# Performance work log

Measured on AMD Instinct MI355X. Metric: run time of the kernel, lower is better.

The kernel has to match this reference:

```python
import jax, jax.numpy as jnp
import numpy as np

N, E, H, D_IN, D_EDGE, L = 20000, 320000, 128, 128, 32, 4
EPS = 1e-5

def setup_inputs() -> dict:
    key = jax.random.key(0)
    ks = jax.random.split(key, 16)
    d_in_edge = 2 * H + 1 + D_EDGE  # cat[h_row, h_col, radial, edge_attr] (input_nf==hidden here)
    s = 0.02
    inp = {
        'h': jax.random.normal(ks[0], (N, D_IN), jnp.float32),
        'coords': jax.random.normal(ks[1], (N, 3), jnp.float32),
        'edge_attr': jax.random.normal(ks[2], (E, D_EDGE), jnp.float32),
        'edges': jax.random.randint(ks[3], (2, E), 0, N),
        'edge_w1': jax.random.normal(ks[4], (L, d_in_edge, H), jnp.float32) * s,
        'edge_b1': jnp.zeros((L, H), jnp.float32),
        'edge_w2': jax.random.normal(ks[5], (L, H, H), jnp.float32) * s,
        'edge_b2': jnp.zeros((L, H), jnp.float32),
        'node_w1': jax.random.normal(ks[6], (L, H + H, H), jnp.float32) * s,
        'node_b1': jnp.zeros((L, H), jnp.float32),
        'node_w2': jax.random.normal(ks[7], (L, H, H), jnp.float32) * s,
        'node_b2': jnp.zeros((L, H), jnp.float32),
        'ln_g': jnp.ones((H,), jnp.float32),
        'ln_b': jnp.zeros((H,), jnp.float32),
    }
    return inp

def _egnn(h, coords, edge_attr, edges, ew1, eb1, ew2, eb2, nw1, nb1, nw2, nb2, ln_g, ln_b):
    row, col = edges[0], edges[1]
    # squared-distance radial feature; coords are not updated across layers
    # (EGNN.forward discards coordinate updates: h, _, _ = layer(...)).
    diff = coords[row] - coords[col]              # [E,3]
    radial = jnp.sum(diff * diff, axis=-1, keepdims=True)  # [E,1]
    for i in range(L):
        hr, hc = h[row], h[col]                   # gathers [E,H]
        m = jnp.concatenate([hr, hc, radial, edge_attr], axis=-1)
        m = jax.nn.silu(m @ ew1[i] + eb1[i])      # [E,H]
        m = jax.nn.silu(m @ ew2[i] + eb2[i])      # [E,H]
        agg = jax.ops.segment_sum(m, row, num_segments=N)  # scatter-add [N,H]
        z = jnp.concatenate([h, agg], axis=-1)    # [N,2H]
        out = jax.nn.silu(z @ nw1[i] + nb1[i]) @ nw2[i] + nb2[i]
        h = out if i == 0 else h + out            # layer 0 non-recurrent
    mu = jnp.mean(h, axis=-1, keepdims=True)
    var = jnp.mean((h - mu) ** 2, axis=-1, keepdims=True)
    return (h - mu) * jax.lax.rsqrt(var + EPS) * ln_g + ln_b

def reference(h, coords, edge_attr, edges, edge_w1, edge_b1, edge_w2, edge_b2,
              node_w1, node_b1, node_w2, node_b2, ln_g, ln_b):
    return _egnn(h, coords, edge_attr, edges, edge_w1, edge_b1, edge_w2, edge_b2,
                 node_w1, node_b1, node_w2, node_b2, ln_g, ln_b)
```

## Files before the change

### kernel.cpp

```cpp
#include <hip/hip_runtime.h>
#include <hip/hip_bf16.h>

#define NN 20000
#define EE 320000
#define HH 128
#define DE 32
#define LL 4

typedef __bf16 bf16_t;
typedef __bf16 bf16x8 __attribute__((ext_vector_type(8)));
typedef __bf16 bf16x4 __attribute__((ext_vector_type(4)));
typedef float f32x4 __attribute__((ext_vector_type(4)));

static __device__ __forceinline__ float silu_f(float x) {
    return x * __builtin_amdgcn_rcpf(1.f + __expf(-x));
}

static __device__ __forceinline__ int permrow(int el) {
    return ((el >> 2) & 3) * 16 + ((el >> 4) & 3) * 4 + (el & 3);
}

__global__ void prep_weights(const float* __restrict__ ew1, const float* __restrict__ eb1f,
                             const float* __restrict__ ew2,
                             const float* __restrict__ nw1, const float* __restrict__ nw2,
                             bf16_t* __restrict__ WPT, bf16_t* __restrict__ W1C,
                             bf16_t* __restrict__ W2T, bf16_t* __restrict__ N1T,
                             bf16_t* __restrict__ N2T)
{
    int i = blockIdx.x * 256 + threadIdx.x;
    const int SW = LL * 256 * 128;
    if (i < SW) {
        int l = i / (256 * 128), r = i % (256 * 128);
        int c = r / 128, k = r % 128;
        int krow = (c < 128) ? k : 128 + k;
        WPT[i] = (bf16_t)ew1[((size_t)l * 289 + krow) * 128 + (c & 127)];
        return;
    }
    i -= SW;
    const int SC = LL * 128 * 64;
    if (i < SC) {
        int l = i / (128 * 64), r = i % (128 * 64);
        int c = r / 64, kk = r % 64;
        float v;
        if (kk == 0)       v = ew1[((size_t)l * 289 + 256) * 128 + c];
        else if (kk <= 32) v = ew1[((size_t)l * 289 + 256 + kk) * 128 + c];
        else if (kk == 33) v = eb1f[l * 128 + c];
        else               v = 0.f;
        W1C[i] = (bf16_t)v;
        return;
    }
    i -= SC;
    const int S2 = LL * 128 * 128;
    if (i < S2) {
        int l = i / (128 * 128), r = i % (128 * 128);
        int n = r / 128, k = r % 128;
        W2T[i] = (bf16_t)ew2[((size_t)l * 128 + k) * 128 + n];
        return;
    }
    i -= S2;
    const int S3 = LL * 128 * 256;
    if (i < S3) {
        int l = i / (128 * 256), r = i % (128 * 256);
        int n = r / 256, k = r % 256;
        N1T[i] = (bf16_t)nw1[((size_t)l * 256 + k) * 128 + n];
        return;
    }
    i -= S3;
    if (i < S2) {
        int l = i / (128 * 128), r = i % (128 * 128);
        int n = r / 128, k = r % 128;
        N2T[i] = (bf16_t)nw2[((size_t)l * 128 + k) * 128 + n];
    }
}

__global__ void hist_kernel(const int* __restrict__ edges, int* __restrict__ counts)
{
    int e = blockIdx.x * 256 + threadIdx.x;
    if (e < EE) atomicAdd(&counts[edges[e]], 1);
}

__global__ void scan_kernel(const int* __restrict__ counts, int* __restrict__ starts)
{
    __shared__ int wsum[16];
    __shared__ int running_s;
    const int tid = threadIdx.x;
    const int lane = tid & 63, wv = tid >> 6;
    if (tid == 0) running_s = 0;
    __syncthreads();
    for (int base = 0; base < NN; base += 1024) {
        int i = base + tid;
        int v = (i < NN) ? counts[i] : 0;
        int orig = v;
        #pragma unroll
        for (int off = 1; off < 64; off <<= 1) {
            int t = __shfl_up(v, off);
            if (lane >= off) v += t;
        }
        if (lane == 63) wsum[wv] = v;
        __syncthreads();
        if (tid < 16) {
            int s = wsum[tid];
            #pragma unroll
            for (int off = 1; off < 16; off <<= 1) {
                int t = __shfl_up(s, off);
                if (tid >= off) s += t;
            }
            wsum[tid] = s;
        }
        __syncthreads();
        int waveoff = (wv == 0) ? 0 : wsum[wv - 1];
        if (i < NN) starts[i] = running_s + waveoff + v - orig;
        int total = wsum[15];
        __syncthreads();
        if (tid == 0) running_s += total;
        __syncthreads();
    }
}

__global__ void scatter_kernel(const int* __restrict__ edges, int* __restrict__ cursor,
                               int* __restrict__ eidx, int* __restrict__ row_s,
                               int* __restrict__ col_s)
{
    int e = blockIdx.x * 256 + threadIdx.x;
    if (e >= EE) return;
    int r = edges[e], c = edges[EE + e];
    int pos = atomicAdd(&cursor[r], 1);
    eidx[pos] = e;
    row_s[pos] = r;
    col_s[pos] = c;
}

__global__ void build_re(const int* __restrict__ eidx, const int* __restrict__ row_s,
                         const int* __restrict__ col_s, const float* __restrict__ coords,
                         const float* __restrict__ ea, bf16_t* __restrict__ RE)
{
    int pos = blockIdx.x * 256 + threadIdx.x;
    if (pos >= EE) return;
    int e = eidx[pos], r = row_s[pos], c = col_s[pos];
    float dx = coords[r * 3 + 0] - coords[c * 3 + 0];
    float dy = coords[r * 3 + 1] - coords[c * 3 + 1];
    float dz = coords[r * 3 + 2] - coords[c * 3 + 2];
    alignas(16) bf16_t buf[40];
    buf[0] = (bf16_t)(dx * dx + dy * dy + dz * dz);
    #pragma unroll
    for (int j = 0; j < 32; ++j) buf[1 + j] = (bf16_t)ea[(size_t)e * DE + j];
    buf[33] = (bf16_t)1.0f;
    #pragma unroll
    for (int j = 34; j < 40; ++j) buf[j] = (bf16_t)0.f;
    bf16x8* dst = (bf16x8*)(RE + (size_t)pos * 40);
    #pragma unroll
    for (int k = 0; k < 5; ++k) dst[k] = ((const bf16x8*)buf)[k];
}

__global__ __launch_bounds__(256, 2) void node_pre(
    const float* __restrict__ h, const bf16_t* __restrict__ WPT,
    bf16_t* __restrict__ P, int layer)
{
    __shared__ bf16_t Hs[64][136];
    const int tid = threadIdx.x;
    const int n0 = blockIdx.x * 64;
    {
        const int nl = tid >> 2, q = tid & 3;
        const int node = n0 + nl;
        if (node < NN) {
            const float* hp = h + (size_t)node * HH;
            #pragma unroll
            for (int j = 0; j < 8; ++j) {
                float4 v = *(const float4*)(hp + q * 32 + j * 4);
                int k = q * 32 + j * 4;
                Hs[nl][k + 0] = (bf16_t)v.x; Hs[nl][k + 1] = (bf16_t)v.y;
                Hs[nl][k + 2] = (bf16_t)v.z; Hs[nl][k + 3] = (bf16_t)v.w;
            }
        } else {
            #pragma unroll
            for (int j = 0; j < 8; ++j) {
                int k = q * 32 + j * 4;
                Hs[nl][k] = (bf16_t)0.f; Hs[nl][k + 1] = (bf16_t)0.f;
                Hs[nl][k + 2] = (bf16_t)0.f; Hs[nl][k + 3] = (bf16_t)0.f;
            }
        }
    }
    __syncthreads();

    const int lane = tid & 63, w = tid >> 6;
    const int ln = lane & 15, kg = lane >> 4;

    f32x4 acc[4][4] = {};
    const bf16_t* Wl = WPT + (size_t)layer * 256 * 128;
    #pragma unroll
    for (int kt = 0; kt < 4; ++kt) {
        const int kb = kt * 32 + kg * 8;
        bf16x8 a[4], b[4];
        #pragma unroll
        for (int m = 0; m < 4; ++m) a[m] = *(const bf16x8*)&Hs[m * 16 + ln][kb];
        #pragma unroll
        for (int n = 0; n < 4; ++n)
            b[n] = *(const bf16x8*)(Wl + (size_t)(w * 64 + n * 16 + ln) * 128 + kb);
        #pragma unroll
        for (int m = 0; m < 4; ++m)
            #pragma unroll
            for (int n = 0; n < 4; ++n)
                acc[m][n] = __builtin_amdgcn_mfma_f32_16x16x32_bf16(a[m], b[n], acc[m][n], 0, 0, 0);
    }
    #pragma unroll
    for (int n = 0; n < 4; ++n) {
        int col = w * 64 + n * 16 + ln;
        #pragma unroll
        for (int m = 0; m < 4; ++m)
            #pragma unroll
            for (int rr = 0; rr < 4; ++rr) {
                int node = n0 + m * 16 + kg * 4 + rr;
                if (node < NN) P[(size_t)node * 256 + col] = (bf16_t)acc[m][n][rr];
            }
    }
}

__global__ __launch_bounds__(256, 6) void edge_kernel(
    const bf16_t* __restrict__ P, const bf16_t* __restrict__ RE,
    const int* __restrict__ row_s, const int* __restrict__ col_s,
    const bf16_t* __restrict__ W1C, const bf16_t* __restrict__ W2T,
    const float* __restrict__ b2, float* __restrict__ agg, int layer)
{
    __shared__ bf16_t pABs[64][136];
    __shared__ bf16_t REb[64][72];

    const int tid = threadIdx.x;
    const int e0 = blockIdx.x * 64;

    {
        const int el = tid >> 2, q = tid & 3;
        const int es = e0 + permrow(el);
        const bf16_t* src = RE + (size_t)es * 40;
        bf16x8 z = {};
        if (q < 2) {
            *(bf16x8*)&REb[el][q * 16]     = *(const bf16x8*)(src + q * 16);
            *(bf16x8*)&REb[el][q * 16 + 8] = *(const bf16x8*)(src + q * 16 + 8);
        } else if (q == 2) {
            *(bf16x8*)&REb[el][32] = *(const bf16x8*)(src + 32);
            *(bf16x8*)&REb[el][40] = z;
        } else {
            *(bf16x8*)&REb[el][48] = z;
            *(bf16x8*)&REb[el][56] = z;
        }
    }
    {
        const int el = tid >> 2, q = tid & 3;
        const int es = e0 + permrow(el);
        int r = row_s[es], c = col_s[es];
        const bf16_t* pa = P + (size_t)r * 256 + q * 32;
        const bf16_t* pb = P + (size_t)c * 256 + 128 + q * 32;
        #pragma unroll
        for (int j = 0; j < 4; ++j) {
            bf16x8 va = *(const bf16x8*)(pa + j * 8);
            bf16x8 vb = *(const bf16x8*)(pb + j * 8);
            bf16x8 o;
            #pragma unroll
            for (int t = 0; t < 8; ++t) o[t] = (bf16_t)((float)va[t] + (float)vb[t]);
            *(bf16x8*)&pABs[el][q * 32 + j * 8] = o;
        }
    }
    __syncthreads();

    const int lane = tid & 63, w = tid >> 6;
    const int ln = lane & 15, kg = lane >> 4;

    f32x4 acc[2][4] = {};
    const bf16_t* W1l = W1C + (size_t)layer * 128 * 64;
    #pragma unroll
    for (int kt = 0; kt < 2; ++kt) {
        const int kb = kt * 32 + kg * 8;
        bf16x8 aW[2], bR[4];
        #pragma unroll
        for (int oc = 0; oc < 2; ++oc)
            aW[oc] = *(const bf16x8*)(W1l + (size_t)(w * 32 + oc * 16 + ln) * 64 + kb);
        #pragma unroll
        for (int e = 0; e < 4; ++e) bR[e] = *(const bf16x8*)&REb[e * 16 + ln][kb];
        #pragma unroll
        for (int oc = 0; oc < 2; ++oc)
            #pragma unroll
            for (int e = 0; e < 4; ++e)
                acc[oc][e] = __builtin_amdgcn_mfma_f32_16x16x32_bf16(aW[oc], bR[e], acc[oc][e], 0, 0, 0);
    }

    #pragma unroll
    for (int oc = 0; oc < 2; ++oc) {
        const int ob = w * 32 + oc * 16 + kg * 4;
        #pragma unroll
        for (int e = 0; e < 4; ++e) {
            const int er = e * 16 + ln;
            bf16x4 pv = *(const bf16x4*)&pABs[er][ob];
            bf16x4 o;
            #pragma unroll
            for (int r = 0; r < 4; ++r)
                o[r] = (bf16_t)silu_f(acc[oc][e][r] + (float)pv[r]);
            *(bf16x4*)&pABs[er][ob] = o;
        }
    }
    __syncthreads();

    f32x4 acc2[4][2] = {};
    const bf16_t* W2l = W2T + (size_t)layer * 128 * 128;
    #pragma unroll
    for (int kt = 0; kt < 4; ++kt) {
        const int kb = kt * 32 + kg * 8;
        bf16x8 a[4], b[2];
        #pragma unroll
        for (int m = 0; m < 4; ++m) a[m] = *(const bf16x8*)&pABs[m * 16 + ln][kb];
        #pragma unroll
        for (int n = 0; n < 2; ++n)
            b[n] = *(const bf16x8*)(W2l + (size_t)(w * 32 + n * 16 + ln) * 128 + kb);
        #pragma unroll
        for (int m = 0; m < 4; ++m)
            #pragma unroll
            for (int n = 0; n < 2; ++n)
                acc2[m][n] = __builtin_amdgcn_mfma_f32_16x16x32_bf16(a[m], b[n], acc2[m][n], 0, 0, 0);
    }

    {
        int myrow[16];
        {
            const int4* rp = (const int4*)(row_s + e0 + kg * 16);
            #pragma unroll
            for (int j = 0; j < 4; ++j) {
                int4 v = rp[j];
                myrow[j * 4 + 0] = v.x; myrow[j * 4 + 1] = v.y;
                myrow[j * 4 + 2] = v.z; myrow[j * 4 + 3] = v.w;
            }
        }

        #pragma unroll
        for (int n = 0; n < 2; ++n) {
            int col = w * 32 + n * 16 + ln;
            float bias = b2[layer * 128 + col];
            float s = 0.f;
            int cur = myrow[0];
            #pragma unroll
            for (int m = 0; m < 4; ++m) {
                #pragma unroll
                for (int rr = 0; rr < 4; ++rr) {
                    int r = myrow[m * 4 + rr];
                    float v = silu_f(acc2[m][n][rr] + bias);
                    if (r != cur) {
                        atomicAdd(&agg[(size_t)cur * HH + col], s);
                        s = 0.f; cur = r;
                    }
                    s += v;
                }
            }
            atomicAdd(&agg[(size_t)cur * HH + col], s);
        }
    }
}

__global__ __launch_bounds__(256, 2) void node_fused(
    const float* __restrict__ hin, float* __restrict__ hout,
    const float* __restrict__ agg,
    const bf16_t* __restrict__ N1T, const float* __restrict__ b1,
    const bf16_t* __restrict__ N2T, const float* __restrict__ b2,
    const bf16_t* __restrict__ WPT, bf16_t* __restrict__ P,
    int layer, int produceP)
{
    __shared__ bf16_t Zs[64][264];
    __shared__ bf16_t M1s[64][136];

    const int tid = threadIdx.x;
    const int n0 = blockIdx.x * 64;

    {
        const int nl = tid >> 2, q = tid & 3;
        const int node = n0 + nl;
        if (node < NN) {
            const float* hp = hin + (size_t)node * HH;
            const float* ap = agg + (size_t)node * HH;
            #pragma unroll
            for (int kk = 0; kk < 64; kk += 4) {
                int k = q * 64 + kk;
                float4 v = (k < 128) ? *(const float4*)(hp + k)
                                     : *(const float4*)(ap + (k - 128));
                Zs[nl][k + 0] = (bf16_t)v.x; Zs[nl][k + 1] = (bf16_t)v.y;
                Zs[nl][k + 2] = (bf16_t)v.z; Zs[nl][k + 3] = (bf16_t)v.w;
            }
        } else {
            #pragma unroll
            for (int kk = 0; kk < 64; kk += 4) {
                int k = q * 64 + kk;
                Zs[nl][k + 0] = (bf16_t)0.f; Zs[nl][k + 1] = (bf16_t)0.f;
                Zs[nl][k + 2] = (bf16_t)0.f; Zs[nl][k + 3] = (bf16_t)0.f;
            }
        }
    }
    __syncthreads();

    const int lane = tid & 63, w = tid >> 6;
    const int ln = lane & 15, kg = lane >> 4;

    f32x4 acc[2][4] = {};
    const bf16_t* N1l = N1T + (size_t)layer * 128 * 256;
    #pragma unroll
    for (int kt = 0; kt < 8; ++kt) {
        const int kb = kt * 32 + kg * 8;
        bf16x8 aW[2], bZ[4];
        #pragma unroll
        for (int oc = 0; oc < 2; ++oc)
            aW[oc] = *(const bf16x8*)(N1l + (size_t)(w * 32 + oc * 16 + ln) * 256 + kb);
        #pragma unroll
        for (int e = 0; e < 4; ++e) bZ[e] = *(const bf16x8*)&Zs[e * 16 + ln][kb];
        #pragma unroll
        for (int oc = 0; oc < 2; ++oc)
            #pragma unroll
            for (int e = 0; e < 4; ++e)
                acc[oc][e] = __builtin_amdgcn_mfma_f32_16x16x32_bf16(aW[oc], bZ[e], acc[oc][e], 0, 0, 0);
    }

    #pragma unroll
    for (int oc = 0; oc < 2; ++oc) {
        const int ob = w * 32 + oc * 16 + kg * 4;
        const float4 b14 = *(const float4*)&b1[layer * 128 + ob];
        #pragma unroll
        for (int e = 0; e < 4; ++e) {
            const int nd = e * 16 + ln;
            bf16x4 o;
            o[0] = (bf16_t)silu_f(acc[oc][e][0] + b14.x);
            o[1] = (bf16_t)silu_f(acc[oc][e][1] + b14.y);
            o[2] = (bf16_t)silu_f(acc[oc][e][2] + b14.z);
            o[3] = (bf16_t)silu_f(acc[oc][e][3] + b14.w);
            *(bf16x4*)&M1s[nd][ob] = o;
        }
    }
    __syncthreads();

    f32x4 acc2[2][4] = {};
    const bf16_t* N2l = N2T + (size_t)layer * 128 * 128;
    #pragma unroll
    for (int kt = 0; kt < 4; ++kt) {
        const int kb = kt * 32 + kg * 8;
        bf16x8 aW[2], bM[4];
        #pragma unroll
        for (int oc = 0; oc < 2; ++oc)
            aW[oc] = *(const bf16x8*)(N2l + (size_t)(w * 32 + oc * 16 + ln) * 128 + kb);
        #pragma unroll
        for (int e = 0; e < 4; ++e) bM[e] = *(const bf16x8*)&M1s[e * 16 + ln][kb];
        #pragma unroll
        for (int oc = 0; oc < 2; ++oc)
            #pragma unroll
            for (int e = 0; e < 4; ++e)
                acc2[oc][e] = __builtin_amdgcn_mfma_f32_16x16x32_bf16(aW[oc], bM[e], acc2[oc][e], 0, 0, 0);
    }

    #pragma unroll
    for (int oc = 0; oc < 2; ++oc) {
        const int ob = w * 32 + oc * 16 + kg * 4;
        const float4 b24 = *(const float4*)&b2[layer * 128 + ob];
        #pragma unroll
        for (int e = 0; e < 4; ++e) {
            const int ndl = e * 16 + ln;
            const int node = n0 + ndl;
            float x0 = acc2[oc][e][0] + b24.x;
            float x1 = acc2[oc][e][1] + b24.y;
            float x2 = acc2[oc][e][2] + b24.z;
            float x3 = acc2[oc][e][3] + b24.w;
            if (node < NN) {
                if (layer != 0) {
                    float4 hv = *(const float4*)&hin[(size_t)node * HH + ob];
                    x0 += hv.x; x1 += hv.y; x2 += hv.z; x3 += hv.w;
                }
                float4 ov; ov.x = x0; ov.y = x1; ov.z = x2; ov.w = x3;
                *(float4*)&hout[(size_t)node * HH + ob] = ov;
            }
            bf16x4 z;
            z[0] = (bf16_t)x0; z[1] = (bf16_t)x1;
            z[2] = (bf16_t)x2; z[3] = (bf16_t)x3;
            *(bf16x4*)&Zs[ndl][ob] = z;
        }
    }

    if (produceP) {
        __syncthreads();
        f32x4 accP[4][4] = {};
        const bf16_t* Wl = WPT + (size_t)(layer + 1) * 256 * 128;
        #pragma unroll
        for (int kt = 0; kt < 4; ++kt) {
            const int kb = kt * 32 + kg * 8;
            bf16x8 aW[4], bZ[4];
            #pragma unroll
            for (int oc = 0; oc < 4; ++oc)
                aW[oc] = *(const bf16x8*)(Wl + (size_t)(w * 64 + oc * 16 + ln) * 128 + kb);
            #pragma unroll
            for (int e = 0; e < 4; ++e) bZ[e] = *(const bf16x8*)&Zs[e * 16 + ln][kb];
            #pragma unroll
            for (int oc = 0; oc < 4; ++oc)
                #pragma unroll
                for (int e = 0; e < 4; ++e)
                    accP[oc][e] = __builtin_amdgcn_mfma_f32_16x16x32_bf16(aW[oc], bZ[e], accP[oc][e], 0, 0, 0);
        }
        #pragma unroll
        for (int oc = 0; oc < 4; ++oc) {
            const int pb = w * 64 + oc * 16 + kg * 4;
            #pragma unroll
            for (int e = 0; e < 4; ++e) {
                const int node = n0 + e * 16 + ln;
                if (node < NN) {
                    bf16x4 o;
                    o[0] = (bf16_t)accP[oc][e][0]; o[1] = (bf16_t)accP[oc][e][1];
                    o[2] = (bf16_t)accP[oc][e][2]; o[3] = (bf16_t)accP[oc][e][3];
                    *(bf16x4*)&P[(size_t)node * 256 + pb] = o;
                }
            }
        }
    }
}

__global__ void ln_kernel(float* __restrict__ h, const float* __restrict__ g,
                          const float* __restrict__ bb)
{
    int node = blockIdx.x * 4 + (threadIdx.x >> 6);
    int lane = threadIdx.x & 63;
    if (node >= NN) return;
    float* hp = h + (size_t)node * HH;
    float v0 = hp[lane], v1 = hp[lane + 64];
    float s = v0 + v1, sq = v0 * v0 + v1 * v1;
    #pragma unroll
    for (int o = 32; o; o >>= 1) {
        s  += __shfl_xor(s, o);
        sq += __shfl_xor(sq, o);
    }
    float mu  = s * (1.f / 128.f);
    float var = sq * (1.f / 128.f) - mu * mu;
    float inv = rsqrtf(var + 1e-5f);
    hp[lane]      = (v0 - mu) * inv * g[lane]      + bb[lane];
    hp[lane + 64] = (v1 - mu) * inv * g[lane + 64] + bb[lane + 64];
}

extern "C" void kernel_launch(void* const* d_in, const int* in_sizes, int n_in,
                              void* d_out, int out_size, void* d_ws, size_t ws_size,
                              hipStream_t stream)
{
    (void)in_sizes; (void)n_in; (void)out_size; (void)ws_size;

    const float* h_in    = (const float*)d_in[0];
    const float* coords  = (const float*)d_in[1];
    const float* ea      = (const float*)d_in[2];
    const int*   edges   = (const int*)d_in[3];
    const float* ew1     = (const float*)d_in[4];
    const float* eb1     = (const float*)d_in[5];
    const float* ew2     = (const float*)d_in[6];
    const float* eb2     = (const float*)d_in[7];
    const float* nw1     = (const float*)d_in[8];
    const float* nb1     = (const float*)d_in[9];
    const float* nw2     = (const float*)d_in[10];
    const float* nb2     = (const float*)d_in[11];
    const float* ln_g    = (const float*)d_in[12];
    const float* ln_b    = (const float*)d_in[13];

    char* ws = (char*)d_ws;
    int*    counts = (int*)(ws + 0);
    int*    starts = (int*)(ws + 80128);
    int*    cursor = (int*)(ws + 160384);
    int*    eidx   = (int*)(ws + 240512);
    int*    row_s  = (int*)(ws + 1520512);
    int*    col_s  = (int*)(ws + 2800512);
    bf16_t* RE     = (bf16_t*)(ws + 4080512);
    bf16_t* P      = (bf16_t*)(ws + 29680512);
    float*  agg    = (float*)(ws + 39920512);
    bf16_t* WPT    = (bf16_t*)(ws + 50160512);
    bf16_t* W1C    = (bf16_t*)(ws + 50422656);
    bf16_t* W2T    = (bf16_t*)(ws + 50488192);
    bf16_t* N1T    = (bf16_t*)(ws + 50619264);
    bf16_t* N2T    = (bf16_t*)(ws + 50881408);

    float* h = (float*)d_out;

    prep_weights<<<1664, 256, 0, stream>>>(ew1, eb1, ew2, nw1, nw2,
                                           WPT, W1C, W2T, N1T, N2T);

    hipMemsetAsync(counts, 0, NN * sizeof(int), stream);
    hist_kernel<<<(EE + 255) / 256, 256, 0, stream>>>(edges, counts);
    scan_kernel<<<1, 1024, 0, stream>>>(counts, starts);
    hipMemcpyAsync(cursor, starts, NN * sizeof(int),
                   hipMemcpyDeviceToDevice, stream);
    scatter_kernel<<<(EE + 255) / 256, 256, 0, stream>>>(edges, cursor, eidx, row_s, col_s);
    build_re<<<(EE + 255) / 256, 256, 0, stream>>>(eidx, row_s, col_s, coords, ea, RE);

    node_pre<<<(NN + 63) / 64, 256, 0, stream>>>(h_in, WPT, P, 0);

    for (int l = 0; l < LL; ++l) {
        hipMemsetAsync(agg, 0, (size_t)NN * HH * sizeof(float), stream);
        edge_kernel<<<EE / 64, 256, 0, stream>>>(P, RE, row_s, col_s,
                                                 W1C, W2T, eb2, agg, l);
        node_fused<<<(NN + 63) / 64, 256, 0, stream>>>(
            (l == 0) ? h_in : h, h, agg, N1T, nb1, N2T, nb2,
            WPT, P, l, (l < LL - 1) ? 1 : 0);
    }
    ln_kernel<<<NN / 4, 256, 0, stream>>>(h, ln_g, ln_b);
}
```

Measured before the change: 432.1 us.

## Load edge gathers directly into MFMA accumulators and halve node tile size

The edge kernel stops staging the gathered P rows and the RE edge features through shared memory. Each lane now loads its P[row]+P[col] slice straight into the accumulator registers as the initial value, and reads RE operands from global memory. This removes a shared-memory staging pass and a barrier, at the cost of narrower (8-byte) uncoalesced gathers and a lower occupancy hint. The node kernel moves from 64 to 32 nodes per block, doubling the grid for more parallelism, and drops its bounds checks because NN divides evenly by 32.

```diff
diff --git a/kernel.cpp b/kernel.cpp
--- a/kernel.cpp
+++ b/kernel.cpp
@@ -14,10 +14,6 @@
 
 static __device__ __forceinline__ float silu_f(float x) {
     return x * __builtin_amdgcn_rcpf(1.f + __expf(-x));
-}
-
-static __device__ __forceinline__ int permrow(int el) {
-    return ((el >> 2) & 3) * 16 + ((el >> 4) & 3) * 4 + (el & 3);
 }
 
 __global__ void prep_weights(const float* __restrict__ ew1, const float* __restrict__ eb1f,
@@ -215,56 +211,41 @@
     }
 }
 
-__global__ __launch_bounds__(256, 6) void edge_kernel(
+__global__ __launch_bounds__(256, 4) void edge_kernel(
     const bf16_t* __restrict__ P, const bf16_t* __restrict__ RE,
     const int* __restrict__ row_s, const int* __restrict__ col_s,
     const bf16_t* __restrict__ W1C, const bf16_t* __restrict__ W2T,
     const float* __restrict__ b2, float* __restrict__ agg, int layer)
 {
-    __shared__ bf16_t pABs[64][136];
-    __shared__ bf16_t REb[64][72];
+    __shared__ bf16_t M1s[64][136];
 
     const int tid = threadIdx.x;
     const int e0 = blockIdx.x * 64;
-
-    {
-        const int el = tid >> 2, q = tid & 3;
-        const int es = e0 + permrow(el);
-        const bf16_t* src = RE + (size_t)es * 40;
-        bf16x8 z = {};
-        if (q < 2) {
-            *(bf16x8*)&REb[el][q * 16]     = *(const bf16x8*)(src + q * 16);
-            *(bf16x8*)&REb[el][q * 16 + 8] = *(const bf16x8*)(src + q * 16 + 8);
-        } else if (q == 2) {
-            *(bf16x8*)&REb[el][32] = *(const bf16x8*)(src + 32);
-            *(bf16x8*)&REb[el][40] = z;
-        } else {
-            *(bf16x8*)&REb[el][48] = z;
-            *(bf16x8*)&REb[el][56] = z;
-        }
-    }
-    {
-        const int el = tid >> 2, q = tid & 3;
-        const int es = e0 + permrow(el);
-        int r = row_s[es], c = col_s[es];
-        const bf16_t* pa = P + (size_t)r * 256 + q * 32;
-        const bf16_t* pb = P + (size_t)c * 256 + 128 + q * 32;
-        #pragma unroll
-        for (int j = 0; j < 4; ++j) {
-            bf16x8 va = *(const bf16x8*)(pa + j * 8);
-            bf16x8 vb = *(const bf16x8*)(pb + j * 8);
-            bf16x8 o;
-            #pragma unroll
-            for (int t = 0; t < 8; ++t) o[t] = (bf16_t)((float)va[t] + (float)vb[t]);
-            *(bf16x8*)&pABs[el][q * 32 + j * 8] = o;
-        }
-    }
-    __syncthreads();
-
     const int lane = tid & 63, w = tid >> 6;
     const int ln = lane & 15, kg = lane >> 4;
 
-    f32x4 acc[2][4] = {};
+    int p[4];
+    #pragma unroll
+    for (int e = 0; e < 4; ++e)
+        p[e] = e0 + ((ln >> 2) * 16) + e * 4 + (ln & 3);
+
+    f32x4 acc[2][4];
+    #pragma unroll
+    for (int e = 0; e < 4; ++e) {
+        int r = row_s[p[e]], c = col_s[p[e]];
+        const bf16_t* pa = P + (size_t)r * 256;
+        const bf16_t* pb = P + (size_t)c * 256 + 128;
+        #pragma unroll
+        for (int oc = 0; oc < 2; ++oc) {
+            const int ob = w * 32 + oc * 16 + kg * 4;
+            bf16x4 va = *(const bf16x4*)(pa + ob);
+            bf16x4 vb = *(const bf16x4*)(pb + ob);
+            #pragma unroll
+            for (int j = 0; j < 4; ++j)
+                acc[oc][e][j] = (float)va[j] + (float)vb[j];
+        }
+    }
+
     const bf16_t* W1l = W1C + (size_t)layer * 128 * 64;
     #pragma unroll
     for (int kt = 0; kt < 2; ++kt) {
@@ -274,7 +255,8 @@
         for (int oc = 0; oc < 2; ++oc)
             aW[oc] = *(const bf16x8*)(W1l + (size_t)(w * 32 + oc * 16 + ln) * 64 + kb);
         #pragma unroll
-        for (int e = 0; e < 4; ++e) bR[e] = *(const bf16x8*)&REb[e * 16 + ln][kb];
+        for (int e = 0; e < 4; ++e)
+            bR[e] = *(const bf16x8*)(RE + (size_t)p[e] * 40 + kb);
         #pragma unroll
         for (int oc = 0; oc < 2; ++oc)
             #pragma unroll
@@ -287,13 +269,11 @@
         const int ob = w * 32 + oc * 16 + kg * 4;
         #pragma unroll
         for (int e = 0; e < 4; ++e) {
-            const int er = e * 16 + ln;
-            bf16x4 pv = *(const bf16x4*)&pABs[er][ob];
             bf16x4 o;
             #pragma unroll
-            for (int r = 0; r < 4; ++r)
-                o[r] = (bf16_t)silu_f(acc[oc][e][r] + (float)pv[r]);
-            *(bf16x4*)&pABs[er][ob] = o;
+            for (int j = 0; j < 4; ++j)
+                o[j] = (bf16_t)silu_f(acc[oc][e][j]);
+            *(bf16x4*)&M1s[e * 16 + ln][ob] = o;
         }
     }
     __syncthreads();
@@ -305,7 +285,7 @@
         const int kb = kt * 32 + kg * 8;
         bf16x8 a[4], b[2];
         #pragma unroll
-        for (int m = 0; m < 4; ++m) a[m] = *(const bf16x8*)&pABs[m * 16 + ln][kb];
+        for (int m = 0; m < 4; ++m) a[m] = *(const bf16x8*)&M1s[m * 16 + ln][kb];
         #pragma unroll
         for (int n = 0; n < 2; ++n)
             b[n] = *(const bf16x8*)(W2l + (size_t)(w * 32 + n * 16 + ln) * 128 + kb);
@@ -352,7 +332,7 @@
     }
 }
 
-__global__ __launch_bounds__(256, 2) void node_fused(
+__global__ __launch_bounds__(256, 4) void node_fused(
     const float* __restrict__ hin, float* __restrict__ hout,
     const float* __restrict__ agg,
     const bf16_t* __restrict__ N1T, const float* __restrict__ b1,
@@ -360,33 +340,24 @@
     const bf16_t* __restrict__ WPT, bf16_t* __restrict__ P,
     int layer, int produceP)
 {
-    __shared__ bf16_t Zs[64][264];
-    __shared__ bf16_t M1s[64][136];
+    __shared__ bf16_t Zs[32][264];
+    __shared__ bf16_t M1s[32][136];
 
     const int tid = threadIdx.x;
-    const int n0 = blockIdx.x * 64;
+    const int n0 = blockIdx.x * 32;
 
     {
-        const int nl = tid >> 2, q = tid & 3;
+        const int nl = tid >> 3, q = tid & 7;
         const int node = n0 + nl;
-        if (node < NN) {
-            const float* hp = hin + (size_t)node * HH;
-            const float* ap = agg + (size_t)node * HH;
-            #pragma unroll
-            for (int kk = 0; kk < 64; kk += 4) {
-                int k = q * 64 + kk;
-                float4 v = (k < 128) ? *(const float4*)(hp + k)
-                                     : *(const float4*)(ap + (k - 128));
-                Zs[nl][k + 0] = (bf16_t)v.x; Zs[nl][k + 1] = (bf16_t)v.y;
-                Zs[nl][k + 2] = (bf16_t)v.z; Zs[nl][k + 3] = (bf16_t)v.w;
-            }
-        } else {
-            #pragma unroll
-            for (int kk = 0; kk < 64; kk += 4) {
-                int k = q * 64 + kk;
-                Zs[nl][k + 0] = (bf16_t)0.f; Zs[nl][k + 1] = (bf16_t)0.f;
-                Zs[nl][k + 2] = (bf16_t)0.f; Zs[nl][k + 3] = (bf16_t)0.f;
-            }
+        const float* hp = hin + (size_t)node * HH;
+        const float* ap = agg + (size_t)node * HH;
+        #pragma unroll
+        for (int kk = 0; kk < 32; kk += 4) {
+            int k = q * 32 + kk;
+            float4 v = (k < 128) ? *(const float4*)(hp + k)
+                                 : *(const float4*)(ap + (k - 128));
+            Zs[nl][k + 0] = (bf16_t)v.x; Zs[nl][k + 1] = (bf16_t)v.y;
+            Zs[nl][k + 2] = (bf16_t)v.z; Zs[nl][k + 3] = (bf16_t)v.w;
         }
     }
     __syncthreads();
@@ -394,21 +365,21 @@
     const int lane = tid & 63, w = tid >> 6;
     const int ln = lane & 15, kg = lane >> 4;
 
-    f32x4 acc[2][4] = {};
+    f32x4 acc[2][2] = {};
     const bf16_t* N1l = N1T + (size_t)layer * 128 * 256;
     #pragma unroll
     for (int kt = 0; kt < 8; ++kt) {
         const int kb = kt * 32 + kg * 8;
-        bf16x8 aW[2], bZ[4];
+        bf16x8 aW[2], bZ[2];
         #pragma unroll
         for (int oc = 0; oc < 2; ++oc)
             aW[oc] = *(const bf16x8*)(N1l + (size_t)(w * 32 + oc * 16 + ln) * 256 + kb);
         #pragma unroll
-        for (int e = 0; e < 4; ++e) bZ[e] = *(const bf16x8*)&Zs[e * 16 + ln][kb];
+        for (int e = 0; e < 2; ++e) bZ[e] = *(const bf16x8*)&Zs[e * 16 + ln][kb];
         #pragma unroll
         for (int oc = 0; oc < 2; ++oc)
             #pragma unroll
-            for (int e = 0; e < 4; ++e)
+            for (int e = 0; e < 2; ++e)
                 acc[oc][e] = __builtin_amdgcn_mfma_f32_16x16x32_bf16(aW[oc], bZ[e], acc[oc][e], 0, 0, 0);
     }
 
@@ -417,7 +388,7 @@
         const int ob = w * 32 + oc * 16 + kg * 4;
         const float4 b14 = *(const float4*)&b1[layer * 128 + ob];
         #pragma unroll
-        for (int e = 0; e < 4; ++e) {
+        for (int e = 0; e < 2; ++e) {
             const int nd = e * 16 + ln;
             bf16x4 o;
             o[0] = (bf16_t)silu_f(acc[oc][e][0] + b14.x);
@@ -429,21 +400,21 @@
     }
     __syncthreads();
 
-    f32x4 acc2[2][4] = {};
+    f32x4 acc2[2][2] = {};
     const bf16_t* N2l = N2T + (size_t)layer * 128 * 128;
     #pragma unroll
     for (int kt = 0; kt < 4; ++kt) {
         const int kb = kt * 32 + kg * 8;
-        bf16x8 aW[2], bM[4];
+        bf16x8 aW[2], bM[2];
         #pragma unroll
         for (int oc = 0; oc < 2; ++oc)
             aW[oc] = *(const bf16x8*)(N2l + (size_t)(w * 32 + oc * 16 + ln) * 128 + kb);
         #pragma unroll
-        for (int e = 0; e < 4; ++e) bM[e] = *(const bf16x8*)&M1s[e * 16 + ln][kb];
+        for (int e = 0; e < 2; ++e) bM[e] = *(const bf16x8*)&M1s[e * 16 + ln][kb];
         #pragma unroll
         for (int oc = 0; oc < 2; ++oc)
             #pragma unroll
-            for (int e = 0; e < 4; ++e)
+            for (int e = 0; e < 2; ++e)
                 acc2[oc][e] = __builtin_amdgcn_mfma_f32_16x16x32_bf16(aW[oc], bM[e], acc2[oc][e], 0, 0, 0);
     }
 
@@ -452,21 +423,19 @@
         const int ob = w * 32 + oc * 16 + kg * 4;
         const float4 b24 = *(const float4*)&b2[layer * 128 + ob];
         #pragma unroll
-        for (int e = 0; e < 4; ++e) {
+        for (int e = 0; e < 2; ++e) {
             const int ndl = e * 16 + ln;
             const int node = n0 + ndl;
             float x0 = acc2[oc][e][0] + b24.x;
             float x1 = acc2[oc][e][1] + b24.y;
             float x2 = acc2[oc][e][2] + b24.z;
             float x3 = acc2[oc][e][3] + b24.w;
-            if (node < NN) {
-                if (layer != 0) {
-                    float4 hv = *(const float4*)&hin[(size_t)node * HH + ob];
-                    x0 += hv.x; x1 += hv.y; x2 += hv.z; x3 += hv.w;
-                }
-                float4 ov; ov.x = x0; ov.y = x1; ov.z = x2; ov.w = x3;
-                *(float4*)&hout[(size_t)node * HH + ob] = ov;
-            }
+            if (layer != 0) {
+                float4 hv = *(const float4*)&hin[(size_t)node * HH + ob];
+                x0 += hv.x; x1 += hv.y; x2 += hv.z; x3 += hv.w;
+            }
+            float4 ov; ov.x = x0; ov.y = x1; ov.z = x2; ov.w = x3;
+            *(float4*)&hout[(size_t)node * HH + ob] = ov;
             bf16x4 z;
             z[0] = (bf16_t)x0; z[1] = (bf16_t)x1;
             z[2] = (bf16_t)x2; z[3] = (bf16_t)x3;
@@ -476,35 +445,33 @@
 
     if (produceP) {
         __syncthreads();
-        f32x4 accP[4][4] = {};
+        f32x4 accP[4][2] = {};
         const bf16_t* Wl = WPT + (size_t)(layer + 1) * 256 * 128;
         #pragma unroll
         for (int kt = 0; kt < 4; ++kt) {
             const int kb = kt * 32 + kg * 8;
-            bf16x8 aW[4], bZ[4];
+            bf16x8 aW[4], bZ[2];
             #pragma unroll
             for (int oc = 0; oc < 4; ++oc)
                 aW[oc] = *(const bf16x8*)(Wl + (size_t)(w * 64 + oc * 16 + ln) * 128 + kb);
             #pragma unroll
-            for (int e = 0; e < 4; ++e) bZ[e] = *(const bf16x8*)&Zs[e * 16 + ln][kb];
+            for (int e = 0; e < 2; ++e) bZ[e] = *(const bf16x8*)&Zs[e * 16 + ln][kb];
             #pragma unroll
             for (int oc = 0; oc < 4; ++oc)
                 #pragma unroll
-                for (int e = 0; e < 4; ++e)
+                for (int e = 0; e < 2; ++e)
                     accP[oc][e] = __builtin_amdgcn_mfma_f32_16x16x32_bf16(aW[oc], bZ[e], accP[oc][e], 0, 0, 0);
         }
         #pragma unroll
         for (int oc = 0; oc < 4; ++oc) {
             const int pb = w * 64 + oc * 16 + kg * 4;
             #pragma unroll
-            for (int e = 0; e < 4; ++e) {
+            for (int e = 0; e < 2; ++e) {
                 const int node = n0 + e * 16 + ln;
-                if (node < NN) {
-                    bf16x4 o;
-                    o[0] = (bf16_t)accP[oc][e][0]; o[1] = (bf16_t)accP[oc][e][1];
-                    o[2] = (bf16_t)accP[oc][e][2]; o[3] = (bf16_t)accP[oc][e][3];
-                    *(bf16x4*)&P[(size_t)node * 256 + pb] = o;
-                }
+                bf16x4 o;
+                o[0] = (bf16_t)accP[oc][e][0]; o[1] = (bf16_t)accP[oc][e][1];
+                o[2] = (bf16_t)accP[oc][e][2]; o[3] = (bf16_t)accP[oc][e][3];
+                *(bf16x4*)&P[(size_t)node * 256 + pb] = o;
             }
         }
     }
@@ -587,7 +554,7 @@
         hipMemsetAsync(agg, 0, (size_t)NN * HH * sizeof(float), stream);
         edge_kernel<<<EE / 64, 256, 0, stream>>>(P, RE, row_s, col_s,
                                                  W1C, W2T, eb2, agg, l);
-        node_fused<<<(NN + 63) / 64, 256, 0, stream>>>(
+        node_fused<<<NN / 32, 256, 0, stream>>>(
             (l == 0) ? h_in : h, h, agg, N1T, nb1, N2T, nb2,
             WPT, P, l, (l < LL - 1) ? 1 : 0);
     }
```

Result: slower. 485.1 us (+12.3%).
